# Kernel tuning notes

Hardware: AMD Instinct MI355X
Metric: run time of the kernel (lower is better)

The kernel has to match this reference:

```python
import jax, jax.numpy as jnp
import numpy as np
from jax import lax

TIME_STEPS = 49          # saves at t = 1..49
STEPS_PER_SAVE = 100     # dt = 0.01 -> 100 Euler steps per unit time
DT = 0.01
B = 8192                 # Monte-Carlo batch
EPS = 1e-7


def setup_inputs() -> dict:
    key = jax.random.key(0)
    condition = jax.random.uniform(key, (B, 4), dtype=jnp.float32)
    return {"condition": condition, "seed": 0}


def _simulate(inf, rec, mr, vol, noise):
    # inf/rec/mr/vol: [B]; noise: [TIME_STEPS, STEPS_PER_SAVE, B] ~ N(0, DT)
    r0_mean = inf / rec
    s0 = jnp.full_like(inf, 0.99)
    i0 = jnp.full_like(inf, 0.01)
    r0_ = jnp.zeros_like(inf)
    y0 = (s0, i0, r0_, r0_mean)  # y0[3] = infection_rate / recovery_rate

    def euler_step(carry, dw):  # dw: [B]
        s, i, r, r0 = carry
        newly_infected = r0 * rec * s
        newly_recovered = rec * i
        s_n = s - DT * newly_infected
        i_n = i + DT * (newly_infected - newly_recovered)
        r_n = r + DT * newly_recovered
        # drift mean-reversion + diffusion scaled by sqrt(|r0|)
        r0_n = r0 + DT * mr * (r0_mean - r0) + jnp.sqrt(jnp.abs(r0)) * vol * dw
        return (s_n, i_n, r_n, r0_n), None

    def save_block(carry, dws):  # dws: [STEPS_PER_SAVE, B]
        carry, _ = lax.scan(euler_step, carry, dws)
        return carry, carry[1]  # save infected fraction at integer times

    _, infected = lax.scan(save_block, y0, noise)  # [TIME_STEPS, B]
    return jnp.nan_to_num(infected, nan=0.0, posinf=0.0, neginf=0.0).T  # [B, T]


def _summarize(x, u):
    # x: [B, TIME_STEPS] infected trajectory, u: [B] uniform
    x = jnp.clip(x, 1e-5)
    max_ = x.max(axis=1)
    max_at = (jnp.argmax(x, axis=1).astype(x.dtype) + u) / TIME_STEPS
    vol = jnp.std(jnp.diff(jnp.log(x), axis=1), axis=1)
    s_loc = jnp.array([0.38, 0.21, 0.14], dtype=x.dtype)
    s_scale = jnp.array([0.14, 0.12, 0.03], dtype=x.dtype)
    s = jnp.stack([max_, max_at, vol], axis=-1)  # [B, 3]
    return (s - s_loc) / s_scale


def reference(condition, seed):
    p = jnp.clip(condition, EPS, 1.0 - EPS)  # [B, 4]
    inf, rec, mr, vol = p[:, 0], p[:, 1], p[:, 2], p[:, 3]
    k_noise, k_u = jax.random.split(jax.random.key(seed))
    noise = jax.random.normal(
        k_noise, (TIME_STEPS, STEPS_PER_SAVE, B), dtype=jnp.float32
    ) * jnp.sqrt(jnp.float32(DT))
    infected = _simulate(inf, rec, mr, vol, noise)  # [B, TIME_STEPS]
    u = jax.random.uniform(k_u, (B,), dtype=jnp.float32)
    return _summarize(infected, u)  # [B, 3]
```

## Files before the change

### kernel.cpp

```cpp
#include <hip/hip_runtime.h>
#include <cstdint>

#pragma clang fp contract(off)

#define TSAVES 49
#define SPSAVE 100
#define NB 8192
#define TRAJ 32
#define GENW 14
#define NDEPTH 6

#define CNTPACK 0x33424442445344ULL

typedef float f32x4 __attribute__((ext_vector_type(4)));

__device__ __forceinline__ uint32_t rotl32(uint32_t v, int d) {
  return __builtin_rotateleft32(v, (uint32_t)d);
}

__device__ __forceinline__ void tf2x32(uint32_t k0, uint32_t k1,
                                       uint32_t x0, uint32_t x1,
                                       uint32_t& o0, uint32_t& o1) {
  uint32_t ks2 = k0 ^ k1 ^ 0x1BD11BDAu;
#define TF_ROUND(r) { x0 += x1; x1 = rotl32(x1, r); x1 ^= x0; }
  x0 += k0; x1 += k1;
  TF_ROUND(13) TF_ROUND(15) TF_ROUND(26) TF_ROUND(6)
  x0 += k1; x1 += ks2 + 1u;
  TF_ROUND(17) TF_ROUND(29) TF_ROUND(16) TF_ROUND(24)
  x0 += ks2; x1 += k0 + 2u;
  TF_ROUND(13) TF_ROUND(15) TF_ROUND(26) TF_ROUND(6)
  x0 += k0; x1 += k1 + 3u;
  TF_ROUND(17) TF_ROUND(29) TF_ROUND(16) TF_ROUND(24)
  x0 += k1; x1 += ks2 + 4u;
  TF_ROUND(13) TF_ROUND(15) TF_ROUND(26) TF_ROUND(6)
  x0 += ks2; x1 += k0 + 5u;
#undef TF_ROUND
  o0 = x0; o1 = x1;
}

__device__ __forceinline__ void derive_keys(int seed, uint32_t& kn0, uint32_t& kn1,
                                            uint32_t& ku0, uint32_t& ku1) {
  uint64_t sv = (uint64_t)(int64_t)seed;
  uint32_t k0 = (uint32_t)(sv >> 32);
  uint32_t k1 = (uint32_t)(sv & 0xffffffffULL);
  tf2x32(k0, k1, 0u, 0u, kn0, kn1);
  tf2x32(k0, k1, 0u, 1u, ku0, ku1);
}

__device__ __forceinline__ uint32_t rand_bits32(uint32_t k0, uint32_t k1, uint32_t n) {
  uint32_t y0, y1;
  tf2x32(k0, k1, 0u, n, y0, y1);
  return y0 ^ y1;
}

__device__ __forceinline__ float bits_to_eu(uint32_t bits) {
#pragma clang fp contract(fast)
  float u01 = __uint_as_float((bits >> 9) | 0x3f800000u) - 1.0f;
  float u = u01 * 2.0f + (-0.99999994f);
  u = fmaxf(-0.99999994f, u);
  float omu2 = 1.0f - u * u;
  float w = -(__builtin_amdgcn_logf(omu2) * 0.6931472f);
  float p;
  if (w < 5.0f) {
    float z = w - 2.5f;
    p = 2.81022636e-08f;
    p = 3.43273939e-07f + p * z;
    p = -3.5233877e-06f + p * z;
    p = -4.39150654e-06f + p * z;
    p = 0.00021858087f + p * z;
    p = -0.00125372503f + p * z;
    p = -0.00417768164f + p * z;
    p = 0.246640727f + p * z;
    p = 1.50140941f + p * z;
  } else {
    float z = __builtin_amdgcn_sqrtf(w) - 3.0f;
    p = -0.000200214257f;
    p = 0.000100950558f + p * z;
    p = 0.00134934322f + p * z;
    p = -0.00367342844f + p * z;
    p = 0.00573950773f + p * z;
    p = -0.0076224613f + p * z;
    p = 0.00943887047f + p * z;
    p = 1.00167406f + p * z;
    p = 2.83297682f + p * z;
  }
  return p * u;
}

__device__ __forceinline__ float clip_param(float x) {
  return fminf(0.99999988f, fmaxf(1e-07f, x));
}

__global__ __launch_bounds__(1024) void fused_kernel(const float* __restrict__ cond,
                                                     const int* __restrict__ seedp,
                                                     float* __restrict__ out) {
  __shared__ f32x4 nbuf[NDEPTH][25][TRAJ];
  __shared__ f32x4 rbuf[2][25][TRAJ];
  __shared__ int done[TSAVES];
  __shared__ int r0cnt, sicnt;

  const int tid = threadIdx.x;
  const int lane = tid & 63;
  const int wv = tid >> 6;
  const int bbase = blockIdx.x * TRAJ;
  const int tr = lane & 31;
  const int h = lane >> 5;
  const int b = bbase + tr;

  if (tid < TSAVES) done[tid] = 0;
  if (tid == 0) { r0cnt = 0; sicnt = 0; }
  __syncthreads();

  volatile int* vdone = done;
  volatile int* vr0 = &r0cnt;
  volatile int* vsi = &sicnt;

  uint32_t kn0, kn1, ku0, ku1;
  derive_keys(seedp[0], kn0, kn1, ku0, ku1);

  float pinf = clip_param(cond[b * 4 + 0]);
  float prec = clip_param(cond[b * 4 + 1]);
  float pmr  = clip_param(cond[b * 4 + 2]);
  float pvol = clip_param(cond[b * 4 + 3]);
  const float r0m  = pinf / prec;
  const float dtmr = 0.01f * pmr;
  const float c4 = 1.0f - dtmr;
  const float a4 = dtmr * r0m;
  const float c2 = 0.01f * prec;
  const float c3 = 1.0f - c2;
  const float c3p4 = (c3 * c3) * (c3 * c3);
  const float cpv = 0.14142136f * pvol;

  if (wv < GENW) {
    const int cnt = (int)((CNTPACK >> (4 * wv)) & 0xFULL);
    int off = 0;
#pragma unroll
    for (int w = 0; w < GENW; ++w) if (w < wv) off += (int)((CNTPACK >> (4 * w)) & 0xFULL);
    for (int g = 0; g <= 48; ++g) {
      if (g >= NDEPTH) {
        while (*vr0 < g - (NDEPTH - 1)) __builtin_amdgcn_s_sleep(1);
      }
      const uint32_t nbase = (uint32_t)(g * SPSAVE) * (uint32_t)NB + (uint32_t)b;
      float* nb = (float*)&nbuf[g % NDEPTH][0][0];
      for (int k = 0; k < cnt; ++k) {
        const int id = off + k;
        const int c = id >> 1;
        const int e = ((id & 1) << 1) | h;
        uint32_t n = nbase + (uint32_t)(4 * c + e) * (uint32_t)NB;
        float eu = bits_to_eu(rand_bits32(kn0, kn1, n));
        nb[(c * 32 + tr) * 4 + e] = eu * cpv;
      }
      __threadfence_block();
      if (lane == 0) atomicAdd(&done[g], 1);
    }
  } else if (wv == GENW) {
    float r0 = r0m;
    for (int g = 0; g <= 48; ++g) {
      while (vdone[g] < GENW) __builtin_amdgcn_s_sleep(1);
      if (g >= 2) {
        while (*vsi < g - 1) __builtin_amdgcn_s_sleep(1);
      }
      __threadfence_block();
      const int sn = g % NDEPTH, sr = g & 1;
      f32x4 vd = nbuf[sn][0][tr];
#pragma unroll
      for (int c = 0; c < 25; ++c) {
        f32x4 vdn = (c < 24) ? nbuf[sn][c + 1][tr] : vd;
        f32x4 w;
#pragma unroll
        for (int e = 0; e < 4; ++e) {
          float sq  = __builtin_amdgcn_sqrtf(fabsf(r0));
          float r0h = fmaf(c4, r0, a4);
          r0 = fmaf(sq, vd[e], r0h);
          w[e] = r0;
        }
        rbuf[sr][c][tr] = w;
        vd = vdn;
      }
      __threadfence_block();
      if (lane == 0) *vr0 = g + 1;
    }
  } else {
    float s = 0.99f, i = 0.01f, r0in = r0m;
    float best = -1.0f; int bi = 0;
    float plg = 0.0f, sd = 0.0f, sd2 = 0.0f;
    for (int g = 0; g <= 48; ++g) {
      while (*vr0 < g + 1) __builtin_amdgcn_s_sleep(1);
      __threadfence_block();
      const int sr = g & 1;
      f32x4 rv = rbuf[sr][0][tr];
#pragma unroll
      for (int c = 0; c < 25; ++c) {
        f32x4 rvn = (c < 24) ? rbuf[sr][c + 1][tr] : rv;
        float rs0 = r0in * s;  s = fmaf(-c2, rs0, s);
        float rs1 = rv[0] * s; s = fmaf(-c2, rs1, s);
        float rs2 = rv[1] * s; s = fmaf(-c2, rs2, s);
        float rs3 = rv[2] * s; s = fmaf(-c2, rs3, s);
        float hh = fmaf(c3, rs0, rs1);
        hh = fmaf(c3, hh, rs2);
        hh = fmaf(c3, hh, rs3);
        i = fmaf(c3p4, i, c2 * hh);
        r0in = rv[3];
        rv = rvn;
      }
      float v = i;
      if (!isfinite(v)) v = 0.0f;
      float x = fmaxf(v, 1e-05f);
      if (x > best) { best = x; bi = g; }
      float lg = __builtin_amdgcn_logf(x) * 0.6931472f;
      if (g > 0) { float d = lg - plg; sd += d; sd2 += d * d; }
      plg = lg;
      __threadfence_block();
      if (lane == 0) *vsi = g + 1;
    }
    if (lane < TRAJ) {
      uint32_t ub = rand_bits32(ku0, ku1, (uint32_t)b);
      float u = __uint_as_float((ub >> 9) | 0x3f800000u) - 1.0f;
      u = fmaxf(0.0f, u);
      float maxat = ((float)bi + u) / 49.0f;
      float mean = sd / 48.0f;
      float var = sd2 / 48.0f - mean * mean;
      float stdv = sqrtf(fmaxf(var, 0.0f));
      out[b * 3 + 0] = (best  - 0.38f) / 0.14f;
      out[b * 3 + 1] = (maxat - 0.21f) / 0.12f;
      out[b * 3 + 2] = (stdv  - 0.14f) / 0.03f;
    }
  }
}

extern "C" void kernel_launch(void* const* d_in, const int* in_sizes, int n_in,
                              void* d_out, int out_size, void* d_ws, size_t ws_size,
                              hipStream_t stream) {
  const float* cond = (const float*)d_in[0];
  const int* seedp = (const int*)d_in[1];
  float* out = (float*)d_out;
  (void)d_ws; (void)ws_size;
  fused_kernel<<<NB / TRAJ, 1024, 0, stream>>>(cond, seedp, out);
}
```

Measured before the change: 131.3 us.

## Merge r0 and SIR consumer waves into one and add a generator wave

The separate r0-diffusion wave and the SIR-integration wave are fused into a single consumer wave, which removes the rbuf shared-memory handoff and its two-way spin-wait synchronisation. The freed wave becomes a fifteenth noise generator, the per-wave work split is rebalanced, and the noise ring buffer grows from 6 to 8 slots. The trade-off is a longer serial dependency chain inside the one consumer wave (sqrt chain plus SIR chain), which may become the critical path, in exchange for less synchronisation and more RNG throughput.

```diff
diff --git a/kernel.cpp b/kernel.cpp
--- a/kernel.cpp
+++ b/kernel.cpp
@@ -7,10 +7,10 @@
 #define SPSAVE 100
 #define NB 8192
 #define TRAJ 32
-#define GENW 14
-#define NDEPTH 6
-
-#define CNTPACK 0x33424442445344ULL
+#define GENW 15
+#define NDEPTH 8
+
+#define CNTPACK 0x333233334443444ULL
 
 typedef float f32x4 __attribute__((ext_vector_type(4)));
 
@@ -95,9 +95,8 @@
                                                      const int* __restrict__ seedp,
                                                      float* __restrict__ out) {
   __shared__ f32x4 nbuf[NDEPTH][25][TRAJ];
-  __shared__ f32x4 rbuf[2][25][TRAJ];
   __shared__ int done[TSAVES];
-  __shared__ int r0cnt, sicnt;
+  __shared__ int simcnt;
 
   const int tid = threadIdx.x;
   const int lane = tid & 63;
@@ -108,12 +107,11 @@
   const int b = bbase + tr;
 
   if (tid < TSAVES) done[tid] = 0;
-  if (tid == 0) { r0cnt = 0; sicnt = 0; }
+  if (tid == 0) simcnt = 0;
   __syncthreads();
 
   volatile int* vdone = done;
-  volatile int* vr0 = &r0cnt;
-  volatile int* vsi = &sicnt;
+  volatile int* vsim = &simcnt;
 
   uint32_t kn0, kn1, ku0, ku1;
   derive_keys(seedp[0], kn0, kn1, ku0, ku1);
@@ -138,7 +136,7 @@
     for (int w = 0; w < GENW; ++w) if (w < wv) off += (int)((CNTPACK >> (4 * w)) & 0xFULL);
     for (int g = 0; g <= 48; ++g) {
       if (g >= NDEPTH) {
-        while (*vr0 < g - (NDEPTH - 1)) __builtin_amdgcn_s_sleep(1);
+        while (*vsim < g - (NDEPTH - 1)) __builtin_amdgcn_s_sleep(1);
       }
       const uint32_t nbase = (uint32_t)(g * SPSAVE) * (uint32_t)NB + (uint32_t)b;
       float* nb = (float*)&nbuf[g % NDEPTH][0][0];
@@ -153,55 +151,40 @@
       __threadfence_block();
       if (lane == 0) atomicAdd(&done[g], 1);
     }
-  } else if (wv == GENW) {
+  } else {
     float r0 = r0m;
+    float s = 0.99f, i = 0.01f;
+    float best = -1.0f; int bi = 0;
+    float plg = 0.0f, sd = 0.0f, sd2 = 0.0f;
     for (int g = 0; g <= 48; ++g) {
       while (vdone[g] < GENW) __builtin_amdgcn_s_sleep(1);
-      if (g >= 2) {
-        while (*vsi < g - 1) __builtin_amdgcn_s_sleep(1);
-      }
       __threadfence_block();
-      const int sn = g % NDEPTH, sr = g & 1;
+      const int sn = g % NDEPTH;
       f32x4 vd = nbuf[sn][0][tr];
 #pragma unroll
       for (int c = 0; c < 25; ++c) {
         f32x4 vdn = (c < 24) ? nbuf[sn][c + 1][tr] : vd;
-        f32x4 w;
-#pragma unroll
-        for (int e = 0; e < 4; ++e) {
-          float sq  = __builtin_amdgcn_sqrtf(fabsf(r0));
-          float r0h = fmaf(c4, r0, a4);
-          r0 = fmaf(sq, vd[e], r0h);
-          w[e] = r0;
-        }
-        rbuf[sr][c][tr] = w;
-        vd = vdn;
-      }
-      __threadfence_block();
-      if (lane == 0) *vr0 = g + 1;
-    }
-  } else {
-    float s = 0.99f, i = 0.01f, r0in = r0m;
-    float best = -1.0f; int bi = 0;
-    float plg = 0.0f, sd = 0.0f, sd2 = 0.0f;
-    for (int g = 0; g <= 48; ++g) {
-      while (*vr0 < g + 1) __builtin_amdgcn_s_sleep(1);
-      __threadfence_block();
-      const int sr = g & 1;
-      f32x4 rv = rbuf[sr][0][tr];
-#pragma unroll
-      for (int c = 0; c < 25; ++c) {
-        f32x4 rvn = (c < 24) ? rbuf[sr][c + 1][tr] : rv;
-        float rs0 = r0in * s;  s = fmaf(-c2, rs0, s);
-        float rs1 = rv[0] * s; s = fmaf(-c2, rs1, s);
-        float rs2 = rv[1] * s; s = fmaf(-c2, rs2, s);
-        float rs3 = rv[2] * s; s = fmaf(-c2, rs3, s);
+        float e0 = r0;
+        { float sq = __builtin_amdgcn_sqrtf(fabsf(r0));
+          float r0h = fmaf(c4, r0, a4); r0 = fmaf(sq, vd[0], r0h); }
+        float e1 = r0;
+        { float sq = __builtin_amdgcn_sqrtf(fabsf(r0));
+          float r0h = fmaf(c4, r0, a4); r0 = fmaf(sq, vd[1], r0h); }
+        float e2 = r0;
+        { float sq = __builtin_amdgcn_sqrtf(fabsf(r0));
+          float r0h = fmaf(c4, r0, a4); r0 = fmaf(sq, vd[2], r0h); }
+        float e3 = r0;
+        { float sq = __builtin_amdgcn_sqrtf(fabsf(r0));
+          float r0h = fmaf(c4, r0, a4); r0 = fmaf(sq, vd[3], r0h); }
+        float rs0 = e0 * s; s = fmaf(-c2, rs0, s);
+        float rs1 = e1 * s; s = fmaf(-c2, rs1, s);
+        float rs2 = e2 * s; s = fmaf(-c2, rs2, s);
+        float rs3 = e3 * s; s = fmaf(-c2, rs3, s);
         float hh = fmaf(c3, rs0, rs1);
         hh = fmaf(c3, hh, rs2);
         hh = fmaf(c3, hh, rs3);
         i = fmaf(c3p4, i, c2 * hh);
-        r0in = rv[3];
-        rv = rvn;
+        vd = vdn;
       }
       float v = i;
       if (!isfinite(v)) v = 0.0f;
@@ -211,7 +194,7 @@
       if (g > 0) { float d = lg - plg; sd += d; sd2 += d * d; }
       plg = lg;
       __threadfence_block();
-      if (lane == 0) *vsi = g + 1;
+      if (lane == 0) *vsim = g + 1;
     }
     if (lane < TRAJ) {
       uint32_t ub = rand_bits32(ku0, ku1, (uint32_t)b);
```

Result: slower. 150.4 us (+14.6%).
